# Kernel tuning notes

Hardware: AMD Instinct MI355X
Metric: run time of the kernel (lower is better)

The kernel has to match this reference:

```python
import jax, jax.numpy as jnp
import numpy as np

B, T, D, H, C, M = 32, 64, 300, 256, 5, 64  # batch, seq, word_dim, rnn_size, classes, n_mention_masks


def _lstm_dir(x, length, W, b, reverse):
    """TF1 LSTMCell (gate order i, j, f, o; forget_bias=1.0) with sequence_length
    semantics of tf.nn.bidirectional_rnn: outputs past length are zero, state is
    copied through. x: [B, T, Din] -> outputs [B, T, H]."""
    Bx, Tx, Din = x.shape
    Hh = b.shape[0] // 4
    xs = jnp.moveaxis(x, 1, 0)                      # [T, B, Din]
    ts = jnp.arange(Tx)
    if reverse:
        xs = xs[::-1]
        ts = Tx - 1 - ts                             # original time index after flip

    def step(carry, inp):
        h, c = carry
        xt, t = inp
        z = jnp.concatenate([xt, h], axis=-1) @ W + b    # [B, 4H]
        i, j, f, o = jnp.split(z, 4, axis=-1)
        c_new = jax.nn.sigmoid(f + 1.0) * c + jax.nn.sigmoid(i) * jnp.tanh(j)
        h_new = jax.nn.sigmoid(o) * jnp.tanh(c_new)
        m = (t < length)[:, None]
        h_out = jnp.where(m, h_new, 0.0)
        return (jnp.where(m, h_new, h), jnp.where(m, c_new, c)), h_out

    init = (jnp.zeros((Bx, Hh), x.dtype), jnp.zeros((Bx, Hh), x.dtype))
    _, outs = jax.lax.scan(step, init, (xs, ts))     # [T, B, H]
    if reverse:
        outs = outs[::-1]
    return jnp.moveaxis(outs, 0, 1)                  # [B, T, H]


def setup_inputs() -> dict:
    key = jax.random.key(0)
    ks = jax.random.split(key, 10)
    def xavier(k, shape):
        fan_in = shape[0]
        return (jax.random.normal(k, shape, jnp.float32) / np.sqrt(fan_in)).astype(jnp.float32)
    return {
        "input_data": jax.random.normal(ks[0], (B, T, D), jnp.float32),
        "entMentIndex": jax.random.uniform(ks[1], (M, B, T, 2 * H), jnp.float32),
        "output_data": jax.random.randint(ks[2], (M // T, T, C), 0, 2, jnp.int32),
        "W_fw": xavier(ks[3], (D + H, 4 * H)),
        "b_fw": jnp.zeros((4 * H,), jnp.float32),
        "W_bw": xavier(ks[4], (D + H, 4 * H)),
        "b_bw": jnp.zeros((4 * H,), jnp.float32),
        "W1": xavier(ks[5], (2 * H, H)),
        "b1": jnp.full((H,), 0.1, jnp.float32),
        "W2": xavier(ks[6], (H, C)),
        "b2": jnp.full((C,), 0.1, jnp.float32),
    }


def reference(input_data, entMentIndex, output_data, W_fw, b_fw, W_bw, b_bw, W1, b1, W2, b2):
    # sequence lengths from non-zero timesteps (all == T for randn inputs)
    used = jnp.sign(jnp.max(jnp.abs(input_data), axis=2))
    length = jnp.sum(used, axis=1).astype(jnp.int32)            # [B]

    out_f = _lstm_dir(input_data, length, W_fw, b_fw, reverse=False)
    out_b = _lstm_dir(input_data, length, W_bw, b_bw, reverse=True)
    output = jnp.concatenate([out_f, out_b], axis=-1)           # [B, T, 2H]

    # tf.scan's lambda ignores the accumulator -> features[m] = output * entMentIndex[m]
    # output_f = mean_T( sum_B( features ) )  ==  einsum / T
    output_f = jnp.einsum('mbtd,btd->md', entMentIndex, output) / T  # [M, 2H]

    l1 = jax.nn.relu(output_f @ W1 + b1)                         # [M, H]
    pred = jax.nn.sigmoid(l1 @ W2 + b2)                          # [M, C]
    prediction = pred.reshape(-1, T, C)                          # [M//T, T, C]

    labels = output_data.astype(prediction.dtype)
    ce = -jnp.sum(labels * jnp.log(prediction), axis=1)          # sum over time
    loss = jnp.mean(ce)
    return prediction, loss
```

## Files before the change

kernel.cpp:

```cpp
#include <hip/hip_runtime.h>
#include <math.h>

#define B_   32
#define T_   64
#define D_   300
#define H_   256
#define G4H  1024
#define M_   64
#define C_   5

typedef _Float16 h2v __attribute__((ext_vector_type(2)));
typedef _Float16 h8  __attribute__((ext_vector_type(8)));
typedef float    f4  __attribute__((ext_vector_type(4)));

__device__ __forceinline__ float sigmoidf_(float x) { return 1.0f / (1.0f + expf(-x)); }

__device__ __forceinline__ float dot2_(h2v a, h2v b, float c) {
#if __has_builtin(__builtin_amdgcn_fdot2)
    return __builtin_amdgcn_fdot2(a, b, c, false);
#else
    return c + (float)a[0] * (float)b[0] + (float)a[1] * (float)b[1];
#endif
}

__global__ void __launch_bounds__(1024)
k_length(const float* __restrict__ x, int* __restrict__ length) {
    const int b   = blockIdx.x;
    const int tid = threadIdx.x;
    const int t   = tid >> 4;
    const int j   = tid & 15;

    __shared__ int cnt;
    if (tid == 0) cnt = 0;
    __syncthreads();

    const float* row = x + (size_t)(b * T_ + t) * D_;
    float mv = 0.f;
    #pragma unroll
    for (int i = 0; i < 19; ++i) {
        int d = j + 16 * i;
        if (d < D_) mv = fmaxf(mv, fabsf(row[d]));
    }
    #pragma unroll
    for (int off = 8; off >= 1; off >>= 1) mv = fmaxf(mv, __shfl_xor(mv, off));
    if (j == 0 && mv > 0.f) atomicAdd(&cnt, 1);
    __syncthreads();
    if (tid == 0) length[b] = cnt;
}

__global__ void __launch_bounds__(256)
k_xw(const float* __restrict__ x,
     const float* __restrict__ Wfw, const float* __restrict__ bfw,
     const float* __restrict__ Wbw, const float* __restrict__ bbw,
     float* __restrict__ xw) {
    const int nt  = blockIdx.x;
    const int mt  = blockIdx.y;
    const int tid = threadIdx.x;
    const int w   = tid >> 6;
    const int l   = tid & 63;
    const int n0  = nt * 128, m0 = mt * 128;
    const int dir = n0 >> 10;
    const float* W    = dir ? Wbw : Wfw;
    const float* bias = dir ? bbw : bfw;
    const int ncol0 = n0 & 1023;

    __shared__ __align__(16) _Float16 As[128][40];
    __shared__ __align__(16) _Float16 Bs[128][40];

    f4 acc[4][4];
    #pragma unroll
    for (int i = 0; i < 4; ++i)
        #pragma unroll
        for (int j = 0; j < 4; ++j) acc[i][j] = (f4){0.f, 0.f, 0.f, 0.f};

    const int wr = (w >> 1) * 64;
    const int wc = (w & 1) * 64;

    for (int k0 = 0; k0 < 320; k0 += 32) {
        #pragma unroll
        for (int p = 0; p < 4; ++p) {
            int row = (tid >> 3) + p * 32;
            int kq  = tid & 7;
            int k   = k0 + kq * 4;
            f4 v = (k < D_) ? *(const f4*)&x[(size_t)(m0 + row) * D_ + k]
                            : (f4){0.f, 0.f, 0.f, 0.f};
            _Float16* dst = &As[row][kq * 4];
            dst[0] = (_Float16)v[0]; dst[1] = (_Float16)v[1];
            dst[2] = (_Float16)v[2]; dst[3] = (_Float16)v[3];
        }
        #pragma unroll
        for (int p = 0; p < 4; ++p) {
            int kk   = (tid >> 5) + p * 8;
            int colq = tid & 31;
            int k    = k0 + kk;
            f4 v = (k < D_) ? *(const f4*)&W[(size_t)k * G4H + ncol0 + colq * 4]
                            : (f4){0.f, 0.f, 0.f, 0.f};
            #pragma unroll
            for (int i = 0; i < 4; ++i) Bs[colq * 4 + i][kk] = (_Float16)v[i];
        }
        __syncthreads();

        h8 afr[4], bfr[4];
        #pragma unroll
        for (int fr = 0; fr < 4; ++fr)
            afr[fr] = *(const h8*)&As[wr + fr * 16 + (l & 15)][(l >> 4) * 8];
        #pragma unroll
        for (int fc = 0; fc < 4; ++fc)
            bfr[fc] = *(const h8*)&Bs[wc + fc * 16 + (l & 15)][(l >> 4) * 8];
        #pragma unroll
        for (int fr = 0; fr < 4; ++fr)
            #pragma unroll
            for (int fc = 0; fc < 4; ++fc)
                acc[fr][fc] = __builtin_amdgcn_mfma_f32_16x16x32_f16(
                    afr[fr], bfr[fc], acc[fr][fc], 0, 0, 0);
        __syncthreads();
    }

    #pragma unroll
    for (int fc = 0; fc < 4; ++fc) {
        int col = ncol0 + wc + fc * 16 + (l & 15);
        float bv = bias[col];
        #pragma unroll
        for (int fr = 0; fr < 4; ++fr) {
            #pragma unroll
            for (int e = 0; e < 4; ++e) {
                int row = m0 + wr + fr * 16 + (l >> 4) * 4 + e;
                xw[(size_t)dir * 2048 * G4H + (size_t)row * G4H + col] =
                    acc[fr][fc][e] + bv;
            }
        }
    }
}

__global__ void __launch_bounds__(512)
k_lstm(const float* __restrict__ Wfw, const float* __restrict__ Wbw,
       const float* __restrict__ xw, const int* __restrict__ length,
       const float* __restrict__ ent, float* __restrict__ partials,
       unsigned* __restrict__ exbuf) {
    const int bid = blockIdx.x;
    const int js  = bid >> 6;
    const int g   = bid & 63;
    const int dir = g >> 5;
    const int b   = g & 31;
    const int tid = threadIdx.x;
    const int w   = tid >> 6;
    const int l   = tid & 63;
    const int c     = w * 32 + (l & 31);
    const int khalf = l >> 5;
    const int colg  = (c >> 6) * 256 + js * 64 + (c & 63);
    const int m8  = tid >> 3;
    const int oct = tid & 7;

    __shared__ __align__(8) _Float16 hl_h[256];
    __shared__ float zfin[256];
    __shared__ float ho_l[64];

    const float* Wg = dir ? Wbw : Wfw;

    h2v wreg[64];
    #pragma unroll
    for (int p = 0; p < 64; ++p) {
        int k = khalf * 128 + 2 * p;
        float w0 = Wg[(size_t)(D_ + k) * G4H + colg];
        float w1 = Wg[(size_t)(D_ + k + 1) * G4H + colg];
        h2v t; t[0] = (_Float16)w0; t[1] = (_Float16)w1;
        wreg[p] = t;
    }

    if (tid < 256) hl_h[tid] = (_Float16)0.f;
    const int len = length[b];
    const size_t xrow = (size_t)(dir * B_ + b) * T_;
    const float* entp = ent + (((size_t)m8 * B_ + b) * T_) * 512
                            + dir * 256 + js * 64 + oct * 8;
    f4 accA = (f4){0.f, 0.f, 0.f, 0.f};
    f4 accB = (f4){0.f, 0.f, 0.f, 0.f};
    __syncthreads();

    float cst = 0.f, hprev = 0.f;

    for (int s = 0; s < T_; ++s) {
        const int tt = dir ? (T_ - 1 - s) : s;
        const unsigned tag = ((unsigned)(s >> 2) & 1u) ^ 1u;
        const size_t slotBase = ((size_t)g * 4 + (s & 3)) * 256;

        f4 e0 = *(const f4*)(entp + (size_t)tt * 512);
        f4 e1 = *(const f4*)(entp + (size_t)tt * 512 + 4);

        float xv = 0.f;
        if (l < 32) xv = xw[(xrow + tt) * G4H + colg];

        float acc = 0.f;
        const uint2* hp = (const uint2*)&hl_h[khalf * 128];
        #pragma unroll
        for (int j = 0; j < 32; ++j) {
            uint2 hv = hp[j];
            acc = dot2_(wreg[2 * j],     __builtin_bit_cast(h2v, hv.x), acc);
            acc = dot2_(wreg[2 * j + 1], __builtin_bit_cast(h2v, hv.y), acc);
        }
        acc += __shfl_xor(acc, 32);
        if (l < 32) zfin[c] = acc + xv;
        __syncthreads();

        if (tid < 64) {
            float zi = zfin[tid], zj = zfin[64 + tid], zf = zfin[128 + tid], zo = zfin[192 + tid];
            float cn = sigmoidf_(zf + 1.0f) * cst + sigmoidf_(zi) * tanhf(zj);
            float hn = sigmoidf_(zo) * tanhf(cn);
            bool  msk = (tt < len);
            float ho  = msk ? hn : 0.f;
            float hk2 = msk ? hn : hprev;
            if (msk) cst = cn;
            hprev = hk2;
            int jglob = js * 64 + tid;
            ho_l[tid] = ho;
            hl_h[jglob] = (_Float16)hk2;
            unsigned bits = (__float_as_uint(hk2) & ~1u) | tag;
            __hip_atomic_store(&exbuf[slotBase + jglob], bits,
                               __ATOMIC_RELAXED, __HIP_MEMORY_SCOPE_AGENT);
        }

        if (tid < 256 && (tid >> 6) != js) {
            unsigned v; unsigned it = 0;
            for (;;) {
                v = __hip_atomic_load(&exbuf[slotBase + tid],
                                      __ATOMIC_RELAXED, __HIP_MEMORY_SCOPE_AGENT);
                if ((v & 1u) == tag) break;
                __builtin_amdgcn_s_sleep(1);
                if (++it > (1u << 20)) break;
            }
            hl_h[tid] = (_Float16)__uint_as_float(v);
        }
        __syncthreads();

        #pragma unroll
        for (int i = 0; i < 4; ++i) {
            accA[i] += e0[i] * ho_l[oct * 8 + i];
            accB[i] += e1[i] * ho_l[oct * 8 + 4 + i];
        }
    }

    float* pp = partials + ((size_t)m8 * B_ + b) * 512 + dir * 256 + js * 64 + oct * 8;
    *(f4*)pp = accA;
    *(f4*)(pp + 4) = accB;
}

__global__ void k_l1(const float* __restrict__ partials, const float* __restrict__ W1,
                     const float* __restrict__ b1, float* __restrict__ l1) {
    const int m = blockIdx.x;
    const int j = threadIdx.x;
    __shared__ float of[512];
    for (int d = j; d < 512; d += 256) {
        float s = 0.f;
        #pragma unroll
        for (int cc = 0; cc < 32; ++cc) s += partials[((size_t)m * B_ + cc) * 512 + d];
        of[d] = s * (1.0f / T_);
    }
    __syncthreads();
    float z = b1[j];
    for (int k = 0; k < 512; ++k) z += of[k] * W1[(size_t)k * H_ + j];
    l1[(size_t)m * H_ + j] = fmaxf(z, 0.f);
}

__global__ void k_head(const float* __restrict__ l1, const float* __restrict__ W2,
                       const float* __restrict__ b2, const int* __restrict__ labels,
                       float* __restrict__ out) {
    const int tid = threadIdx.x;
    __shared__ float red[320];
    float term = 0.f;
    if (tid < 320) {
        int m = tid / 5, cc = tid % 5;
        float z = b2[cc];
        for (int k = 0; k < H_; ++k) z += l1[(size_t)m * H_ + k] * W2[(size_t)k * C_ + cc];
        float p = 1.f / (1.f + expf(-z));
        out[tid] = p;
        term = -(float)labels[tid] * logf(p);
    }
    red[tid] = term;
    __syncthreads();
    if (tid == 0) {
        float s = 0.f;
        for (int i = 0; i < 320; ++i) s += red[i];
        out[320] = s / (float)C_;
    }
}

extern "C" void kernel_launch(void* const* d_in, const int* in_sizes, int n_in,
                              void* d_out, int out_size, void* d_ws, size_t ws_size,
                              hipStream_t stream) {
    const float* x      = (const float*)d_in[0];
    const float* ent    = (const float*)d_in[1];
    const int*   labels = (const int*)d_in[2];
    const float* Wfw    = (const float*)d_in[3];
    const float* bfw    = (const float*)d_in[4];
    const float* Wbw    = (const float*)d_in[5];
    const float* bbw    = (const float*)d_in[6];
    const float* W1     = (const float*)d_in[7];
    const float* b1     = (const float*)d_in[8];
    const float* W2     = (const float*)d_in[9];
    const float* b2     = (const float*)d_in[10];
    float* out = (float*)d_out;

    float*    ws       = (float*)d_ws;
    float*    xw       = ws;
    unsigned* exbuf    = (unsigned*)(xw + 4194304);
    float*    l1       = (float*)(exbuf + 65536);
    int*      length   = (int*)(l1 + 16384);
    float*    partials = (float*)(length + 32);

    k_length<<<32, 1024, 0, stream>>>(x, length);
    k_xw<<<dim3(16, 16), 256, 0, stream>>>(x, Wfw, bfw, Wbw, bbw, xw);
    k_lstm<<<256, 512, 0, stream>>>(Wfw, Wbw, xw, length, ent, partials, exbuf);
    k_l1<<<64, 256, 0, stream>>>(partials, W1, b1, l1);
    k_head<<<1, 320, 0, stream>>>(l1, W2, b2, labels, out);
}
```

Before: 204.3 us.

## Offload entity-mention reduction to consumer blocks polling a full per-step h history

```diff
diff --git a/kernel.cpp b/kernel.cpp
--- a/kernel.cpp
+++ b/kernel.cpp
@@ -21,6 +21,12 @@
 #else
     return c + (float)a[0] * (float)b[0] + (float)a[1] * (float)b[1];
 #endif
+}
+
+__global__ void k_zero(unsigned* __restrict__ p, int n4) {
+    int idx = blockIdx.x * blockDim.x + threadIdx.x;
+    uint4 z = {0u, 0u, 0u, 0u};
+    if (idx < n4) ((uint4*)p)[idx] = z;
 }
 
 __global__ void __launch_bounds__(1024)
@@ -133,127 +139,139 @@
 }
 
 __global__ void __launch_bounds__(512)
-k_lstm(const float* __restrict__ Wfw, const float* __restrict__ Wbw,
+k_main(const float* __restrict__ Wfw, const float* __restrict__ Wbw,
        const float* __restrict__ xw, const int* __restrict__ length,
-       const float* __restrict__ ent, float* __restrict__ partials,
+       const float* __restrict__ ent, float* __restrict__ outf,
        unsigned* __restrict__ exbuf) {
-    const int bid = blockIdx.x;
-    const int js  = bid >> 6;
-    const int g   = bid & 63;
-    const int dir = g >> 5;
-    const int b   = g & 31;
     const int tid = threadIdx.x;
-    const int w   = tid >> 6;
-    const int l   = tid & 63;
-    const int c     = w * 32 + (l & 31);
-    const int khalf = l >> 5;
-    const int colg  = (c >> 6) * 256 + js * 64 + (c & 63);
-    const int m8  = tid >> 3;
-    const int oct = tid & 7;
-
-    __shared__ __align__(8) _Float16 hl_h[256];
-    __shared__ float zfin[256];
-    __shared__ float ho_l[64];
-
-    const float* Wg = dir ? Wbw : Wfw;
-
-    h2v wreg[64];
-    #pragma unroll
-    for (int p = 0; p < 64; ++p) {
-        int k = khalf * 128 + 2 * p;
-        float w0 = Wg[(size_t)(D_ + k) * G4H + colg];
-        float w1 = Wg[(size_t)(D_ + k + 1) * G4H + colg];
-        h2v t; t[0] = (_Float16)w0; t[1] = (_Float16)w1;
-        wreg[p] = t;
-    }
-
-    if (tid < 256) hl_h[tid] = (_Float16)0.f;
-    const int len = length[b];
-    const size_t xrow = (size_t)(dir * B_ + b) * T_;
-    const float* entp = ent + (((size_t)m8 * B_ + b) * T_) * 512
-                            + dir * 256 + js * 64 + oct * 8;
-    f4 accA = (f4){0.f, 0.f, 0.f, 0.f};
-    f4 accB = (f4){0.f, 0.f, 0.f, 0.f};
-    __syncthreads();
-
-    float cst = 0.f, hprev = 0.f;
-
-    for (int s = 0; s < T_; ++s) {
-        const int tt = dir ? (T_ - 1 - s) : s;
-        const unsigned tag = ((unsigned)(s >> 2) & 1u) ^ 1u;
-        const size_t slotBase = ((size_t)g * 4 + (s & 3)) * 256;
-
-        f4 e0 = *(const f4*)(entp + (size_t)tt * 512);
-        f4 e1 = *(const f4*)(entp + (size_t)tt * 512 + 4);
-
-        float xv = 0.f;
-        if (l < 32) xv = xw[(xrow + tt) * G4H + colg];
-
-        float acc = 0.f;
-        const uint2* hp = (const uint2*)&hl_h[khalf * 128];
-        #pragma unroll
-        for (int j = 0; j < 32; ++j) {
-            uint2 hv = hp[j];
-            acc = dot2_(wreg[2 * j],     __builtin_bit_cast(h2v, hv.x), acc);
-            acc = dot2_(wreg[2 * j + 1], __builtin_bit_cast(h2v, hv.y), acc);
-        }
-        acc += __shfl_xor(acc, 32);
-        if (l < 32) zfin[c] = acc + xv;
+
+    if (blockIdx.x < 256) {
+        const int bid = blockIdx.x;
+        const int js  = bid >> 6;
+        const int g   = bid & 63;
+        const int dir = g >> 5;
+        const int b   = g & 31;
+        const int w   = tid >> 6;
+        const int l   = tid & 63;
+        const int c     = w * 32 + (l & 31);
+        const int khalf = l >> 5;
+        const int colg  = (c >> 6) * 256 + js * 64 + (c & 63);
+
+        __shared__ __align__(8) _Float16 hl_h[256];
+        __shared__ float zfin[256];
+
+        const float* Wg = dir ? Wbw : Wfw;
+
+        h2v wreg[64];
+        #pragma unroll
+        for (int p = 0; p < 64; ++p) {
+            int k = khalf * 128 + 2 * p;
+            float w0 = Wg[(size_t)(D_ + k) * G4H + colg];
+            float w1 = Wg[(size_t)(D_ + k + 1) * G4H + colg];
+            h2v t; t[0] = (_Float16)w0; t[1] = (_Float16)w1;
+            wreg[p] = t;
+        }
+
+        if (tid < 256) hl_h[tid] = (_Float16)0.f;
+        const int len = length[b];
+        const size_t xrow = (size_t)(dir * B_ + b) * T_;
         __syncthreads();
 
-        if (tid < 64) {
-            float zi = zfin[tid], zj = zfin[64 + tid], zf = zfin[128 + tid], zo = zfin[192 + tid];
-            float cn = sigmoidf_(zf + 1.0f) * cst + sigmoidf_(zi) * tanhf(zj);
-            float hn = sigmoidf_(zo) * tanhf(cn);
-            bool  msk = (tt < len);
-            float ho  = msk ? hn : 0.f;
-            float hk2 = msk ? hn : hprev;
-            if (msk) cst = cn;
-            hprev = hk2;
-            int jglob = js * 64 + tid;
-            ho_l[tid] = ho;
-            hl_h[jglob] = (_Float16)hk2;
-            unsigned bits = (__float_as_uint(hk2) & ~1u) | tag;
-            __hip_atomic_store(&exbuf[slotBase + jglob], bits,
-                               __ATOMIC_RELAXED, __HIP_MEMORY_SCOPE_AGENT);
-        }
-
-        if (tid < 256 && (tid >> 6) != js) {
+        float cst = 0.f, hprev = 0.f;
+
+        for (int s = 0; s < T_; ++s) {
+            const int tt = dir ? (T_ - 1 - s) : s;
+            const size_t slotBase = ((size_t)g * 64 + s) * 256;
+
+            float xv = 0.f;
+            if (l < 32) xv = xw[(xrow + tt) * G4H + colg];
+
+            float acc = 0.f;
+            const uint2* hp = (const uint2*)&hl_h[khalf * 128];
+            #pragma unroll
+            for (int j = 0; j < 32; ++j) {
+                uint2 hv = hp[j];
+                acc = dot2_(wreg[2 * j],     __builtin_bit_cast(h2v, hv.x), acc);
+                acc = dot2_(wreg[2 * j + 1], __builtin_bit_cast(h2v, hv.y), acc);
+            }
+            acc += __shfl_xor(acc, 32);
+            if (l < 32) zfin[c] = acc + xv;
+            __syncthreads();
+
+            if (tid < 64) {
+                float zi = zfin[tid], zj = zfin[64 + tid];
+                float zf = zfin[128 + tid], zo = zfin[192 + tid];
+                float cn = sigmoidf_(zf + 1.0f) * cst + sigmoidf_(zi) * tanhf(zj);
+                float hn = sigmoidf_(zo) * tanhf(cn);
+                bool  msk = (tt < len);
+                float hk2 = msk ? hn : hprev;
+                if (msk) cst = cn;
+                hprev = hk2;
+                int jglob = js * 64 + tid;
+                hl_h[jglob] = (_Float16)hk2;
+                unsigned bits = (__float_as_uint(hk2) & ~1u) | 1u;
+                __hip_atomic_store(&exbuf[slotBase + jglob], bits,
+                                   __ATOMIC_RELAXED, __HIP_MEMORY_SCOPE_AGENT);
+            }
+
+            if (tid < 256 && (tid >> 6) != js) {
+                unsigned v; unsigned it = 0;
+                for (;;) {
+                    v = __hip_atomic_load(&exbuf[slotBase + tid],
+                                          __ATOMIC_RELAXED, __HIP_MEMORY_SCOPE_AGENT);
+                    if (v & 1u) break;
+                    __builtin_amdgcn_s_sleep(1);
+                    if (++it > (1u << 22)) break;
+                }
+                hl_h[tid] = (_Float16)__uint_as_float(v);
+            }
+            __syncthreads();
+        }
+    } else {
+        const int cid = blockIdx.x - 256;
+        const int mg  = cid >> 5;
+        const int b   = cid & 31;
+        const int d   = tid;
+        const int half = d >> 8;
+        const int g    = half ? (32 + b) : b;
+        const int col  = d & 255;
+        const int len  = length[b];
+
+        float acc[8] = {};
+
+        for (int s = 0; s < T_; ++s) {
+            const int t = half ? (T_ - 1 - s) : s;
+            if (t >= len) continue;
+
+            const size_t slotBase = ((size_t)g * 64 + s) * 256;
             unsigned v; unsigned it = 0;
             for (;;) {
-                v = __hip_atomic_load(&exbuf[slotBase + tid],
+                v = __hip_atomic_load(&exbuf[slotBase + col],
                                       __ATOMIC_RELAXED, __HIP_MEMORY_SCOPE_AGENT);
-                if ((v & 1u) == tag) break;
+                if (v & 1u) break;
                 __builtin_amdgcn_s_sleep(1);
-                if (++it > (1u << 20)) break;
-            }
-            hl_h[tid] = (_Float16)__uint_as_float(v);
-        }
-        __syncthreads();
-
-        #pragma unroll
-        for (int i = 0; i < 4; ++i) {
-            accA[i] += e0[i] * ho_l[oct * 8 + i];
-            accB[i] += e1[i] * ho_l[oct * 8 + 4 + i];
-        }
-    }
-
-    float* pp = partials + ((size_t)m8 * B_ + b) * 512 + dir * 256 + js * 64 + oct * 8;
-    *(f4*)pp = accA;
-    *(f4*)(pp + 4) = accB;
-}
-
-__global__ void k_l1(const float* __restrict__ partials, const float* __restrict__ W1,
+                if (++it > (1u << 22)) break;
+            }
+            float h = __uint_as_float(v);
+
+            #pragma unroll
+            for (int i = 0; i < 8; ++i)
+                acc[i] += ent[(((size_t)(mg * 8 + i) * B_ + b) * T_ + t) * 512 + d] * h;
+        }
+
+        #pragma unroll
+        for (int i = 0; i < 8; ++i)
+            atomicAdd(&outf[(mg * 8 + i) * 512 + d], acc[i]);
+    }
+}
+
+__global__ void k_l1(const float* __restrict__ outf, const float* __restrict__ W1,
                      const float* __restrict__ b1, float* __restrict__ l1) {
     const int m = blockIdx.x;
     const int j = threadIdx.x;
     __shared__ float of[512];
-    for (int d = j; d < 512; d += 256) {
-        float s = 0.f;
-        #pragma unroll
-        for (int cc = 0; cc < 32; ++cc) s += partials[((size_t)m * B_ + cc) * 512 + d];
-        of[d] = s * (1.0f / T_);
-    }
+    for (int d = j; d < 512; d += 256)
+        of[d] = outf[(size_t)m * 512 + d] * (1.0f / T_);
     __syncthreads();
     float z = b1[j];
     for (int k = 0; k < 512; ++k) z += of[k] * W1[(size_t)k * H_ + j];
@@ -299,16 +317,18 @@
     const float* b2     = (const float*)d_in[10];
     float* out = (float*)d_out;
 
-    float*    ws       = (float*)d_ws;
-    float*    xw       = ws;
-    unsigned* exbuf    = (unsigned*)(xw + 4194304);
-    float*    l1       = (float*)(exbuf + 65536);
-    int*      length   = (int*)(l1 + 16384);
-    float*    partials = (float*)(length + 32);
-
+    float*    ws     = (float*)d_ws;
+    float*    xw     = ws;
+    unsigned* exbuf  = (unsigned*)(xw + 4194304);
+    float*    outf   = (float*)(exbuf + 1048576);
+    float*    l1     = outf + 32768;
+    int*      length = (int*)(l1 + 16384);
+
+    const int n4 = 270336;
+    k_zero<<<(n4 + 255) / 256, 256, 0, stream>>>(exbuf, n4);
     k_length<<<32, 1024, 0, stream>>>(x, length);
     k_xw<<<dim3(16, 16), 256, 0, stream>>>(x, Wfw, bfw, Wbw, bbw, xw);
-    k_lstm<<<256, 512, 0, stream>>>(Wfw, Wbw, xw, length, ent, partials, exbuf);
-    k_l1<<<64, 256, 0, stream>>>(partials, W1, b1, l1);
+    k_main<<<512, 512, 0, stream>>>(Wfw, Wbw, xw, length, ent, outf, exbuf);
+    k_l1<<<64, 256, 0, stream>>>(outf, W1, b1, l1);
     k_head<<<1, 320, 0, stream>>>(l1, W2, b2, labels, out);
 }
```

New measurement: 240.2 us. +17.6%, slower.
